# Kernel optimization log

Measured on AMD Instinct MI355X. Metric: run time of the kernel, lower is better.

Reference implementation:

```python
import jax, jax.numpy as jnp
import numpy as np
from jax import lax

MAXD = 192 // 4 + 1  # 49 disparity hypotheses
BN_EPS = 1e-5
LEAKY_SLOPE = 0.01


def setup_inputs() -> dict:
    key = jax.random.key(0)
    ks = jax.random.split(key, 8)
    b, c, h, w = 4, 96, 160, 320
    hid = 96
    return {
        "imL": jax.random.normal(ks[0], (b, c, h, w), jnp.float32),
        "imR": jax.random.normal(ks[1], (b, c, h, w), jnp.float32),
        "conv_w": jax.random.normal(ks[2], (hid, c, 3, 3), jnp.float32) * 0.05,
        "bn_gamma": jnp.ones((hid,), jnp.float32),
        "bn_beta": jnp.zeros((hid,), jnp.float32),
        "bn_mean": jax.random.normal(ks[3], (hid,), jnp.float32) * 0.1,
        "bn_var": jax.random.uniform(ks[4], (hid,), jnp.float32, 0.5, 1.5),
        "desc_w": jax.random.normal(ks[5], (hid, hid), jnp.float32) * 0.1,
        "desc_b": jax.random.normal(ks[6], (hid,), jnp.float32) * 0.01,
    }


def _features(im, conv_w, bn_gamma, bn_beta, bn_mean, bn_var, desc_w, desc_b):
    # BasicConv: 3x3 conv (no bias) + BatchNorm (inference stats) + LeakyReLU
    z = lax.conv_general_dilated(im, conv_w, (1, 1), "SAME",
                                 dimension_numbers=("NCHW", "OIHW", "NCHW"))
    scale = bn_gamma / jnp.sqrt(bn_var + BN_EPS)
    z = z * scale[None, :, None, None] + (bn_beta - bn_mean * scale)[None, :, None, None]
    z = jnp.where(z >= 0, z, LEAKY_SLOPE * z)
    # desc: 1x1 conv with bias
    d = jnp.einsum("bchw,oc->bohw", z, desc_w) + desc_b[None, :, None, None]
    # L2-normalize over channels (matches x_/torch.norm(x_,2,1,True))
    n = jnp.sqrt(jnp.sum(d * d, axis=1, keepdims=True))
    return d / n


def reference(imL, imR, conv_w, bn_gamma, bn_beta, bn_mean, bn_var, desc_w, desc_b):
    x = _features(imL, conv_w, bn_gamma, bn_beta, bn_mean, bn_var, desc_w, desc_b)
    y = _features(imR, conv_w, bn_gamma, bn_beta, bn_mean, bn_var, desc_w, desc_b)
    b, c, h, w = x.shape
    costs = [jnp.sum(x * y, axis=1)]  # [b,h,w], disparity 0
    for i in range(1, MAXD):
        corr = jnp.sum(x[:, :, :, i:] * y[:, :, :, : w - i], axis=1)  # [b,h,w-i]
        costs.append(jnp.pad(corr, ((0, 0), (0, 0), (i, 0))))
    # torch cats [1,b,h,w] tensors along dim 1 -> [1, D*b, h, w], then unsqueeze(0)
    cost = jnp.stack(costs, axis=0).reshape(1, 1, MAXD * b, h, w)
    return cost
```

## Files before the change

kernel.cpp:

```cpp
#include <hip/hip_runtime.h>
#include <hip/hip_bf16.h>

#define BATCH 4
#define CH    96
#define HH    160
#define WW    320
#define MAXD  49
#define BN_EPS 1e-5f
#define SLOPE  0.01f

typedef __attribute__((ext_vector_type(8))) short bf16x8;
typedef __attribute__((ext_vector_type(4))) float f32x4;

__device__ __forceinline__ ushort f2b(float f) {
    __hip_bfloat16 h = __float2bfloat16(f);
    return *reinterpret_cast<ushort*>(&h);
}

__launch_bounds__(256)
__global__ void transpose_kernel(const float* __restrict__ imL,
                                 const float* __restrict__ imR,
                                 short* __restrict__ imT)
{
    __shared__ ushort tile[96 * 74];
    const int t  = threadIdx.x;
    const int x0 = blockIdx.x * 64;
    const int y  = blockIdx.y;
    const int z  = blockIdx.z;
    const int b = z & 3, img = z >> 2;
    const float* __restrict__ im = img ? imR : imL;
    for (int e = t; e < 96 * 64; e += 256) {
        int ci = e >> 6, x = e & 63;
        tile[ci * 74 + x] = f2b(im[((b * CH + ci) * HH + y) * WW + x0 + x]);
    }
    __syncthreads();
    short* __restrict__ out = imT + (((size_t)z * HH + y) * WW + x0) * CH;
    for (int e = t; e < 64 * 96; e += 256) {
        int x = e / 96, ci = e - x * 96;
        out[e] = (short)tile[ci * 74 + x];
    }
}

__launch_bounds__(256)
__global__ void pack_kernel(const float* __restrict__ conv_w,
                            const float* __restrict__ bn_gamma,
                            const float* __restrict__ bn_beta,
                            const float* __restrict__ bn_mean,
                            const float* __restrict__ bn_var,
                            const float* __restrict__ desc_w,
                            short* __restrict__ packW,
                            short* __restrict__ packD,
                            float* __restrict__ shv)
{
    int id = blockIdx.x * 256 + threadIdx.x;
    if (id < 82944) {
        int j = id & 7, l = (id >> 3) & 63;
        int rest = id >> 9;
        int mf = rest % 6; int r2 = rest / 6;
        int tp = r2 % 9;  int chunk = r2 / 9;
        int co = mf * 16 + (l & 15);
        int ci = chunk * 32 + ((l >> 4) << 3) + j;
        float sc = bn_gamma[co] / sqrtf(bn_var[co] + BN_EPS);
        packW[id] = (short)f2b(conv_w[(co * 96 + ci) * 9 + tp] * sc);
    } else if (id < 92160) {
        int d = id - 82944;
        int j = d & 7, l = (d >> 3) & 63;
        int rest = d >> 9;
        int mf = rest % 6, s2 = rest / 6;
        int o = mf * 16 + (l & 15);
        int c = s2 * 32 + ((l >> 4) << 3) + j;
        packD[d] = (short)f2b(desc_w[o * 96 + c]);
    } else if (id < 92256) {
        int co = id - 92160;
        float sc = bn_gamma[co] / sqrtf(bn_var[co] + BN_EPS);
        shv[co] = bn_beta[co] - bn_mean[co] * sc;
    }
}

__launch_bounds__(256, 3)
__global__ void feat_mfma_kernel(const short* __restrict__ imT,
                                 const short* __restrict__ packW,
                                 const short* __restrict__ packD,
                                 const float* __restrict__ shv,
                                 const float* __restrict__ desc_b,
                                 short* __restrict__ feat)
{
    __shared__ __align__(16) short lds[16384];

    const int tid  = threadIdx.x;
    const int lane = tid & 63, w = tid >> 6;
    const int q = lane >> 4, l15 = lane & 15;
    const int x0 = blockIdx.x * 32, y0 = blockIdx.y * 4;
    const int z  = blockIdx.z;
    const size_t imbase = (size_t)z * HH * WW * CH;

    const bf16x8 vz8 = {0, 0, 0, 0, 0, 0, 0, 0};
    const f32x4  fz  = {0.f, 0.f, 0.f, 0.f};

    f32x4 acc[6][2];
#pragma unroll
    for (int mf = 0; mf < 6; ++mf) { acc[mf][0] = fz; acc[mf][1] = fz; }

    const bf16x8* __restrict__ wv = (const bf16x8*)packW;
    bf16x8 sv[4];

#define STAGE_LOAD(chunk)                                                      \
    {                                                                          \
        _Pragma("unroll")                                                      \
        for (int k = 0; k < 4; ++k) {                                          \
            int e = tid + k * 256;                                             \
            bf16x8 v = vz8;                                                    \
            if (e < 816) {                                                     \
                int r = e / 136, rem = e - r * 136;                            \
                int cc = rem >> 2, g = rem & 3;                                \
                int gy = y0 - 1 + r, gx = x0 - 1 + cc;                         \
                if ((unsigned)gy < HH && (unsigned)gx < WW)                    \
                    v = *(const bf16x8*)(imT + imbase +                        \
                        ((size_t)gy * WW + gx) * CH + (chunk) * 32 + g * 8);   \
            }                                                                  \
            sv[k] = v;                                                         \
        }                                                                      \
    }

#define STAGE_WRITE(bufofs)                                                    \
    {                                                                          \
        _Pragma("unroll")                                                      \
        for (int k = 0; k < 4; ++k) {                                          \
            int e = tid + k * 256;                                             \
            if (e < 816) {                                                     \
                int r = e / 136, rem = e - r * 136;                            \
                int cc = rem >> 2, g = rem & 3;                                \
                *(bf16x8*)&lds[(bufofs) + (r * 34 + cc) * 40 + g * 8] = sv[k]; \
            }                                                                  \
        }                                                                      \
    }

    STAGE_LOAD(0);
    STAGE_WRITE(0);
    __syncthreads();

#pragma unroll
    for (int c = 0; c < 3; ++c) {
        if (c < 2) STAGE_LOAD(c + 1);
        const int bo = (c & 1) ? 8160 : 0;
        for (int tp = 0; tp < 9; ++tp) {
            int dy = tp / 3, dx = tp - dy * 3;
            int cell = (w + dy) * 34 + l15 + dx;
            bf16x8 B0 = *(const bf16x8*)&lds[bo + cell * 40 + q * 8];
            bf16x8 B1 = *(const bf16x8*)&lds[bo + (cell + 16) * 40 + q * 8];
            const bf16x8* wf = wv + ((c * 9 + tp) * 6) * 64 + lane;
#pragma unroll
            for (int mf = 0; mf < 6; ++mf) {
                bf16x8 A = wf[mf * 64];
                acc[mf][0] = __builtin_amdgcn_mfma_f32_16x16x32_bf16(A, B0, acc[mf][0], 0, 0, 0);
                acc[mf][1] = __builtin_amdgcn_mfma_f32_16x16x32_bf16(A, B1, acc[mf][1], 0, 0, 0);
            }
        }
        if (c < 2) {
            STAGE_WRITE((c & 1) ? 0 : 8160);
            __syncthreads();
        }
    }
    __syncthreads();

    short* zs = lds + w * 4096;

#pragma unroll
    for (int mf = 0; mf < 6; ++mf)
#pragma unroll
        for (int p = 0; p < 2; ++p) {
            int pix = p * 16 + l15;
#pragma unroll
            for (int r = 0; r < 4; r += 2) {
                int co = mf * 16 + q * 4 + r;
                float z0 = acc[mf][p][r]     + shv[co];
                float z1 = acc[mf][p][r + 1] + shv[co + 1];
                z0 = z0 >= 0.f ? z0 : SLOPE * z0;
                z1 = z1 >= 0.f ? z1 : SLOPE * z1;
                unsigned pk = (unsigned)f2b(z0) | ((unsigned)f2b(z1) << 16);
                int c8 = mf * 2 + (q >> 1);
                int zi = pix * 128 + ((c8 ^ l15) * 8) + (q & 1) * 4 + r;
                *(unsigned*)&zs[zi] = pk;
            }
        }

    f32x4 dacc[6][2];
#pragma unroll
    for (int mf = 0; mf < 6; ++mf) { dacc[mf][0] = fz; dacc[mf][1] = fz; }
    const bf16x8* __restrict__ dv = (const bf16x8*)packD;
#pragma unroll
    for (int s2 = 0; s2 < 3; ++s2) {
        int ch16 = s2 * 4 + q;
        bf16x8 B0 = *(const bf16x8*)&zs[l15 * 128        + ((ch16 ^ l15) * 8)];
        bf16x8 B1 = *(const bf16x8*)&zs[(16 + l15) * 128 + ((ch16 ^ l15) * 8)];
        const bf16x8* df = dv + (s2 * 6) * 64 + lane;
#pragma unroll
        for (int mf = 0; mf < 6; ++mf) {
            bf16x8 A = df[mf * 64];
            dacc[mf][0] = __builtin_amdgcn_mfma_f32_16x16x32_bf16(A, B0, dacc[mf][0], 0, 0, 0);
            dacc[mf][1] = __builtin_amdgcn_mfma_f32_16x16x32_bf16(A, B1, dacc[mf][1], 0, 0, 0);
        }
    }

    float ss0 = 0.f, ss1 = 0.f;
#pragma unroll
    for (int mf = 0; mf < 6; ++mf)
#pragma unroll
        for (int r = 0; r < 4; ++r) {
            int o = mf * 16 + q * 4 + r;
            float bias = desc_b[o];
            float d0 = dacc[mf][0][r] + bias;
            float d1 = dacc[mf][1][r] + bias;
            dacc[mf][0][r] = d0; dacc[mf][1][r] = d1;
            ss0 += d0 * d0; ss1 += d1 * d1;
        }
    ss0 += __shfl_xor(ss0, 16, 64); ss0 += __shfl_xor(ss0, 32, 64);
    ss1 += __shfl_xor(ss1, 16, 64); ss1 += __shfl_xor(ss1, 32, 64);
    const float rn0 = 1.f / sqrtf(ss0), rn1 = 1.f / sqrtf(ss1);

#pragma unroll
    for (int mf = 0; mf < 6; ++mf)
#pragma unroll
        for (int p = 0; p < 2; ++p) {
            int pix = p * 16 + l15;
            float rn = p ? rn1 : rn0;
#pragma unroll
            for (int r = 0; r < 4; r += 2) {
                float d0 = dacc[mf][p][r]     * rn;
                float d1 = dacc[mf][p][r + 1] * rn;
                unsigned pk = (unsigned)f2b(d0) | ((unsigned)f2b(d1) << 16);
                int c8 = mf * 2 + (q >> 1);
                int zi = pix * 128 + ((c8 ^ l15) * 8) + (q & 1) * 4 + r;
                *(unsigned*)&zs[zi] = pk;
            }
        }

    short* __restrict__ fo = feat + (((size_t)z * HH + y0 + w) * WW + x0) * CH;
#pragma unroll
    for (int it = 0; it < 6; ++it) {
        int cid = it * 64 + lane;
        int pix = cid / 12, c16 = cid - pix * 12;
        bf16x8 v = *(const bf16x8*)&zs[pix * 128 + ((c16 ^ (pix & 15)) * 8)];
        *(bf16x8*)&fo[pix * 96 + c16 * 8] = v;
    }
#undef STAGE_LOAD
#undef STAGE_WRITE
}

#define NCOL 368
#define YPITCH 104
__launch_bounds__(256, 2)
__global__ void cost_mfma_kernel(const short* __restrict__ xF,
                                 const short* __restrict__ yF,
                                 float* __restrict__ out)
{
    __shared__ __align__(16) short ylds[NCOL * YPITCH];
    const int tid = threadIdx.x, lane = tid & 63, w = tid >> 6;
    const int q = lane >> 4, l15 = lane & 15;
    const int y = blockIdx.x, b = blockIdx.y;

    const bf16x8 vz8 = {0, 0, 0, 0, 0, 0, 0, 0};
    const f32x4  fz  = {0.f, 0.f, 0.f, 0.f};

    for (int e = tid; e < 624; e += 256)
        *(bf16x8*)&ylds[e * 8] = vz8;

    const size_t ybase = ((size_t)(4 + b) * HH + y) * WW * CH;
    for (int wl = w; wl < 65; wl += 4) {
        int cb  = 624 + wl * 64;
        int cid = cb + lane;
        int col = cid / 13, ch = cid - col * 13;
        if (ch == 12) ch = 0;
        const short* gp = yF + ybase + (size_t)(col - 48) * CH + ch * 8;
        __builtin_amdgcn_global_load_lds(
            (const __attribute__((address_space(1))) unsigned int*)gp,
            (__attribute__((address_space(3))) unsigned int*)&ylds[(size_t)cb * 8],
            16, 0, 0);
    }
    __syncthreads();

    const size_t xbase = ((size_t)b * HH + y) * WW * CH;
    const int T0 = w * 5;

    bf16x8 Bc[4][3];
#pragma unroll
    for (int u = 0; u < 4; ++u)
#pragma unroll
        for (int s2 = 0; s2 < 3; ++s2)
            Bc[u][s2] = *(const bf16x8*)&ylds[(16 * (T0 + u) + l15) * YPITCH
                                              + (s2 * 4 + q) * 8];

#pragma unroll
    for (int tl = 0; tl < 5; ++tl) {
        bf16x8 A[3];
#pragma unroll
        for (int s2 = 0; s2 < 3; ++s2)
            A[s2] = *(const bf16x8*)(xF + xbase +
                     (size_t)(16 * (T0 + tl) + l15) * 96 + s2 * 32 + q * 8);
        if (tl > 0) {
#pragma unroll
            for (int s2 = 0; s2 < 3; ++s2)
                Bc[(tl + 3) & 3][s2] = *(const bf16x8*)&ylds[
                    (16 * (T0 + tl + 3) + l15) * YPITCH + (s2 * 4 + q) * 8];
        }
        f32x4 acc[4] = {fz, fz, fz, fz};
#pragma unroll
        for (int u = 0; u < 4; ++u)
#pragma unroll
            for (int s2 = 0; s2 < 3; ++s2)
                acc[u] = __builtin_amdgcn_mfma_f32_16x16x32_bf16(
                    A[s2], Bc[(tl + u) & 3][s2], acc[u], 0, 0, 0);

        const int x = 16 * (T0 + tl) + q * 4;
#pragma unroll
        for (int u = 0; u < 4; ++u)
#pragma unroll
            for (int r = 0; r < 4; ++r) {
                int d = 48 - 16 * u + q * 4 + r - l15;
                if (0 <= d && d <= 48)
                    out[((size_t)(d * BATCH + b) * HH + y) * WW + x + r] = acc[u][r];
            }
    }
}

extern "C" void kernel_launch(void* const* d_in, const int* in_sizes, int n_in,
                              void* d_out, int out_size, void* d_ws, size_t ws_size,
                              hipStream_t stream)
{
    const float* imL      = (const float*)d_in[0];
    const float* imR      = (const float*)d_in[1];
    const float* conv_w   = (const float*)d_in[2];
    const float* bn_gamma = (const float*)d_in[3];
    const float* bn_beta  = (const float*)d_in[4];
    const float* bn_mean  = (const float*)d_in[5];
    const float* bn_var   = (const float*)d_in[6];
    const float* desc_w   = (const float*)d_in[7];
    const float* desc_b   = (const float*)d_in[8];

    const size_t half = (size_t)8 * HH * WW * CH;
    short* imT  = (short*)d_ws;
    short* feat = (short*)d_ws + half;

    short* packW = (short*)d_out;
    short* packD = (short*)((char*)d_out + 165888);
    float* shv   = (float*)((char*)d_out + 184320);

    dim3 tgrid(WW / 64, HH, 2 * BATCH);
    transpose_kernel<<<tgrid, 256, 0, stream>>>(imL, imR, imT);

    pack_kernel<<<361, 256, 0, stream>>>(conv_w, bn_gamma, bn_beta, bn_mean,
                                         bn_var, desc_w, packW, packD, shv);

    dim3 fgrid(WW / 32, HH / 4, 2 * BATCH);
    feat_mfma_kernel<<<fgrid, 256, 0, stream>>>(imT, packW, packD, shv,
                                                desc_b, feat);

    dim3 cgrid(HH, BATCH);
    cost_mfma_kernel<<<cgrid, 256, 0, stream>>>(feat, feat, (float*)d_out);
}
```

Baseline: 395.4 us.

## Split cost kernel into 64-column tiles and stage output through LDS

The cost-volume kernel is now split across five 64-column tiles per row, which shrinks the LDS footprint and raises the occupancy bound from 2 to 4. Each block stages its 49x64 cost tile in LDS and writes it out as contiguous row segments, replacing the old scattered per-lane stores. Boundary zeroing is done only in the first column tile. The feature-conv tap loop is also fully unrolled. The cost is extra barriers and reloading the 48-column halo for every tile.

```diff
diff --git a/kernel.cpp b/kernel.cpp
--- a/kernel.cpp
+++ b/kernel.cpp
@@ -143,6 +143,7 @@
     for (int c = 0; c < 3; ++c) {
         if (c < 2) STAGE_LOAD(c + 1);
         const int bo = (c & 1) ? 8160 : 0;
+#pragma unroll
         for (int tp = 0; tp < 9; ++tp) {
             int dy = tp / 3, dx = tp - dy * 3;
             int cell = (w + dy) * 34 + l15 + dx;
@@ -247,31 +248,40 @@
 #undef STAGE_WRITE
 }
 
-#define NCOL 368
-#define YPITCH 104
-__launch_bounds__(256, 2)
+__launch_bounds__(256, 4)
 __global__ void cost_mfma_kernel(const short* __restrict__ xF,
                                  const short* __restrict__ yF,
                                  float* __restrict__ out)
 {
-    __shared__ __align__(16) short ylds[NCOL * YPITCH];
+    __shared__ __align__(16) char smem[23552];
+    short* ylds  = (short*)smem;
+    float* otile = (float*)smem;
+
     const int tid = threadIdx.x, lane = tid & 63, w = tid >> 6;
     const int q = lane >> 4, l15 = lane & 15;
-    const int y = blockIdx.x, b = blockIdx.y;
+    const int bx = blockIdx.x, y = blockIdx.y, b = blockIdx.z;
+    const int X0 = bx * 64;
 
     const bf16x8 vz8 = {0, 0, 0, 0, 0, 0, 0, 0};
     const f32x4  fz  = {0.f, 0.f, 0.f, 0.f};
 
-    for (int e = tid; e < 624; e += 256)
-        *(bf16x8*)&ylds[e * 8] = vz8;
+    const size_t xbase = ((size_t)b * HH + y) * WW * CH;
+    bf16x8 Af[3];
+#pragma unroll
+    for (int s2 = 0; s2 < 3; ++s2)
+        Af[s2] = *(const bf16x8*)(xF + xbase +
+                 (size_t)(X0 + 16 * w + l15) * CH + s2 * 32 + q * 8);
 
     const size_t ybase = ((size_t)(4 + b) * HH + y) * WW * CH;
-    for (int wl = w; wl < 65; wl += 4) {
-        int cb  = 624 + wl * 64;
+    for (int wl = w; wl < 23; wl += 4) {
+        int cb  = wl * 64;
         int cid = cb + lane;
-        int col = cid / 13, ch = cid - col * 13;
+        int c2  = cid < 1456 ? cid : 1455;
+        int col = c2 / 13, ch = c2 - col * 13;
         if (ch == 12) ch = 0;
-        const short* gp = yF + ybase + (size_t)(col - 48) * CH + ch * 8;
+        int xp = X0 - 48 + col;
+        if (xp < 0) xp = 0;
+        const short* gp = yF + ybase + (size_t)xp * CH + ch * 8;
         __builtin_amdgcn_global_load_lds(
             (const __attribute__((address_space(1))) unsigned int*)gp,
             (__attribute__((address_space(3))) unsigned int*)&ylds[(size_t)cb * 8],
@@ -279,47 +289,42 @@
     }
     __syncthreads();
 
-    const size_t xbase = ((size_t)b * HH + y) * WW * CH;
-    const int T0 = w * 5;
-
-    bf16x8 Bc[4][3];
-#pragma unroll
-    for (int u = 0; u < 4; ++u)
+    if (bx == 0) {
+        for (int e = tid; e < 624; e += 256)
+            *(bf16x8*)&ylds[e * 8] = vz8;
+        __syncthreads();
+    }
+
+    bf16x8 Bf[4][3];
+#pragma unroll
+    for (int g = 0; g < 4; ++g)
 #pragma unroll
         for (int s2 = 0; s2 < 3; ++s2)
-            Bc[u][s2] = *(const bf16x8*)&ylds[(16 * (T0 + u) + l15) * YPITCH
+            Bf[g][s2] = *(const bf16x8*)&ylds[(16 * (w + g) + l15) * 104
                                               + (s2 * 4 + q) * 8];
-
-#pragma unroll
-    for (int tl = 0; tl < 5; ++tl) {
-        bf16x8 A[3];
+    __syncthreads();
+
+    f32x4 acc[4] = {fz, fz, fz, fz};
+#pragma unroll
+    for (int g = 0; g < 4; ++g)
 #pragma unroll
         for (int s2 = 0; s2 < 3; ++s2)
-            A[s2] = *(const bf16x8*)(xF + xbase +
-                     (size_t)(16 * (T0 + tl) + l15) * 96 + s2 * 32 + q * 8);
-        if (tl > 0) {
-#pragma unroll
-            for (int s2 = 0; s2 < 3; ++s2)
-                Bc[(tl + 3) & 3][s2] = *(const bf16x8*)&ylds[
-                    (16 * (T0 + tl + 3) + l15) * YPITCH + (s2 * 4 + q) * 8];
-        }
-        f32x4 acc[4] = {fz, fz, fz, fz};
-#pragma unroll
-        for (int u = 0; u < 4; ++u)
-#pragma unroll
-            for (int s2 = 0; s2 < 3; ++s2)
-                acc[u] = __builtin_amdgcn_mfma_f32_16x16x32_bf16(
-                    A[s2], Bc[(tl + u) & 3][s2], acc[u], 0, 0, 0);
-
-        const int x = 16 * (T0 + tl) + q * 4;
-#pragma unroll
-        for (int u = 0; u < 4; ++u)
-#pragma unroll
-            for (int r = 0; r < 4; ++r) {
-                int d = 48 - 16 * u + q * 4 + r - l15;
-                if (0 <= d && d <= 48)
-                    out[((size_t)(d * BATCH + b) * HH + y) * WW + x + r] = acc[u][r];
-            }
+            acc[g] = __builtin_amdgcn_mfma_f32_16x16x32_bf16(Af[s2], Bf[g][s2],
+                                                             acc[g], 0, 0, 0);
+
+#pragma unroll
+    for (int g = 0; g < 4; ++g)
+#pragma unroll
+        for (int r = 0; r < 4; ++r) {
+            int d = 48 - 16 * g + q * 4 + r - l15;
+            if (0 <= d && d <= 48)
+                otile[d * 73 + 16 * w + q * 4 + r] = acc[g][r];
+        }
+    __syncthreads();
+
+    for (int e = tid; e < 49 * 64; e += 256) {
+        int d = e >> 6, xl = e & 63;
+        out[((size_t)(d * BATCH + b) * HH + y) * WW + X0 + xl] = otile[d * 73 + xl];
     }
 }
 
@@ -355,6 +360,6 @@
     feat_mfma_kernel<<<fgrid, 256, 0, stream>>>(imT, packW, packD, shv,
                                                 desc_b, feat);
 
-    dim3 cgrid(HH, BATCH);
+    dim3 cgrid(5, HH, BATCH);
     cost_mfma_kernel<<<cgrid, 256, 0, stream>>>(feat, feat, (float*)d_out);
 }
```

New measurement: 380.2 us. 1.04x faster.
